# Performance work log

Hardware: AMD Instinct MI355X
Metric: run time of the kernel (lower is better)

Reference implementation:

```python
import jax, jax.numpy as jnp
import numpy as np

N_NODES = 100_000
N_EDGES = 600_000
D = 128


def setup_inputs() -> dict:
    key = jax.random.key(0)
    ks = jax.random.split(key, 8)
    x = jax.random.normal(ks[0], (N_NODES, D), dtype=jnp.float32)
    edge_index = jax.random.randint(ks[1], (2, N_EDGES), 0, N_NODES, dtype=jnp.int32)
    s = 1.0 / np.sqrt(D)
    Wn = jax.random.normal(ks[2], (D, D), dtype=jnp.float32) * s
    bn = jax.random.normal(ks[3], (D,), dtype=jnp.float32) * s
    We = jax.random.normal(ks[4], (D, 2 * D), dtype=jnp.float32) * s
    be = jax.random.normal(ks[5], (D,), dtype=jnp.float32) * s
    Wu = jax.random.normal(ks[6], (D, 3 * D), dtype=jnp.float32) * s
    bu = jax.random.normal(ks[7], (D,), dtype=jnp.float32) * s
    return {"x": x, "edge_index": edge_index, "Wn": Wn, "bn": bn,
            "We": We, "be": be, "Wu": Wu, "bu": bu}


def reference(x, edge_index, Wn, bn, We, be, Wu, bu):
    # x: [N, D] node embeddings; edge_index: [2, E]
    n = x.shape[0]
    src, dst = edge_index[0], edge_index[1]
    # node linear: [N, D]
    node_emb = x @ Wn.T + bn
    # edge linear on concatenated endpoint embeddings: [E, D]
    edge_in = jnp.concatenate([x[src], x[dst]], axis=1)  # [E, 2D]
    edge_emb = edge_in @ We.T + be
    # scatter-add neighbor node embeddings and edge embeddings into source nodes
    agg_node = jax.ops.segment_sum(node_emb[dst], src, num_segments=n)  # [N, D]
    agg_edge = jax.ops.segment_sum(edge_emb, src, num_segments=n)       # [N, D]
    pre = jnp.concatenate([node_emb, agg_node, agg_edge], axis=1)       # [N, 3D]
    # exact (erf) GELU matches torch nn.GELU default
    return jax.nn.gelu(pre, approximate=False) @ Wu.T + bu
```

## Files before the change

kernel.cpp:

```cpp
#include <hip/hip_runtime.h>
#include <hip/hip_bf16.h>
#include <math.h>

#define NNODES 100000
#define NEDGES 600000
#define DD 128
#define SCAN_B 512
#define NFRAGS 6250
#define TGRID 512

typedef __attribute__((ext_vector_type(8))) short bf16x8;
typedef __attribute__((ext_vector_type(4))) float f32x4;
typedef __attribute__((ext_vector_type(4))) unsigned short u16x4;

static __device__ __forceinline__ unsigned short f2bf(float f) {
    __hip_bfloat16 h = __float2bfloat16(f);
    return __builtin_bit_cast(unsigned short, h);
}
static __device__ __forceinline__ float bf2f(unsigned short h) {
    unsigned u = ((unsigned)h) << 16;
    return __builtin_bit_cast(float, u);
}
static __device__ __forceinline__ float gelu_fast(float v) {
    float w = v * (-2.302203846f - 0.102943150f * v * v);
#if __has_builtin(__builtin_amdgcn_exp2f)
    float e = __builtin_amdgcn_exp2f(w);
#else
    float e = exp2f(w);
#endif
#if __has_builtin(__builtin_amdgcn_rcpf)
    return v * __builtin_amdgcn_rcpf(1.0f + e);
#else
    return v / (1.0f + e);
#endif
}

#if __has_builtin(__builtin_amdgcn_global_load_lds)
#define HAVE_GLDS 1
#else
#define HAVE_GLDS 0
#endif

static __device__ __forceinline__ void gload_lds16(const unsigned short* g, unsigned short* s, int lane) {
#if HAVE_GLDS
    (void)lane;
    __builtin_amdgcn_global_load_lds((const __attribute__((address_space(1))) void*)g,
                                     (__attribute__((address_space(3))) void*)s, 16, 0, 0);
#else
    *(bf16x8*)(s + lane * 8) = *(const bf16x8*)g;
#endif
}
static __device__ __forceinline__ void gload_lds4(const float* g, unsigned short* s, int lane) {
#if HAVE_GLDS
    (void)lane;
    __builtin_amdgcn_global_load_lds((const __attribute__((address_space(1))) void*)g,
                                     (__attribute__((address_space(3))) void*)s, 4, 0, 0);
#else
    *(float*)((char*)s + lane * 4) = *g;
#endif
}

#define MFMA(a, b, c) __builtin_amdgcn_mfma_f32_16x16x32_bf16(a, b, c, 0, 0, 0)
#define BARX() do { asm volatile("s_waitcnt lgkmcnt(0)" ::: "memory"); \
                    __builtin_amdgcn_s_barrier(); } while (0)

template <int LAYOUT>
__global__ __launch_bounds__(256) void prep_k(const float* __restrict__ x,
                                              const float* __restrict__ Wn,
                                              const float* __restrict__ We,
                                              const float* __restrict__ Wu,
                                              unsigned short* __restrict__ wfrag,
                                              int* __restrict__ cnt,
                                              unsigned short* __restrict__ xb) {
    int b = blockIdx.x;
    int t = threadIdx.x;
    if (b < 48) {
        int tid = b * 256 + t;
        int l = tid & 63;
        const float* src;
        if constexpr (LAYOUT == 0) {
            int ct = (tid >> 6) & 7;
            int kt = (tid >> 9) & 3;
            int tile = tid >> 11;
            int n = ct * 16 + (l & 15);
            int k = kt * 32 + (l >> 4) * 8;
            switch (tile) {
                case 0:  src = Wn + (size_t)n * 128 + k;        break;
                case 1:  src = Wu + (size_t)n * 384 + k;        break;
                case 2:  src = We + (size_t)n * 256 + k;        break;
                case 3:  src = We + (size_t)n * 256 + 128 + k;  break;
                case 4:  src = Wu + (size_t)n * 384 + 128 + k;  break;
                default: src = Wu + (size_t)n * 384 + 256 + k;  break;
            }
        } else {
            int g = tid >> 6;
            int l16 = l & 15, lg8 = (l >> 4) * 8;
            if (g < 32)       { int nf = g >> 2,        kt = g & 3;
                                src = Wn + (size_t)(nf * 16 + l16) * 128 + kt * 32 + lg8; }
            else if (g < 64)  { int gg = g - 32; int nf = gg >> 2, kt = gg & 3;
                                src = We + (size_t)(nf * 16 + l16) * 256 + kt * 32 + lg8; }
            else if (g < 96)  { int gg = g - 64; int nf = gg >> 2, kt = gg & 3;
                                src = We + (size_t)(nf * 16 + l16) * 256 + 128 + kt * 32 + lg8; }
            else              { int gg = g - 96; int nf = gg / 12, kt = gg % 12;
                                src = Wu + (size_t)(nf * 16 + l16) * 384 + kt * 32 + lg8; }
        }
        unsigned short o[8];
#pragma unroll
        for (int j = 0; j < 8; ++j) o[j] = f2bf(src[j]);
        *(bf16x8*)(wfrag + (size_t)(b * 256 + t) * 8) = *(bf16x8*)o;
    } else if (b < 48 + 391) {
        int i = (b - 48) * 256 + t;
        if (i < NNODES) cnt[i] = 0;
    } else {
        int i = (b - 439) * 256 + t;
        float4 v0 = *(const float4*)(x + (size_t)i * 8);
        float4 v1 = *(const float4*)(x + (size_t)i * 8 + 4);
        unsigned short o[8] = { f2bf(v0.x), f2bf(v0.y), f2bf(v0.z), f2bf(v0.w),
                                f2bf(v1.x), f2bf(v1.y), f2bf(v1.z), f2bf(v1.w) };
        *(bf16x8*)(xb + (size_t)i * 8) = *(bf16x8*)o;
    }
}

__global__ __launch_bounds__(256) void hist_k(const int* __restrict__ ei, int* __restrict__ cnt) {
    int e = blockIdx.x * 256 + threadIdx.x;
    if (e < NEDGES) atomicAdd(&cnt[ei[e]], 1);
}

__global__ __launch_bounds__(SCAN_B) void scan_local(const int* __restrict__ cnt,
                                                     int* __restrict__ off,
                                                     int* __restrict__ bsum) {
    __shared__ int sh[SCAN_B];
    int i = blockIdx.x * SCAN_B + threadIdx.x;
    int v = (i < NNODES) ? cnt[i] : 0;
    sh[threadIdx.x] = v;
    __syncthreads();
    for (int d = 1; d < SCAN_B; d <<= 1) {
        int t = (threadIdx.x >= d) ? sh[threadIdx.x - d] : 0;
        __syncthreads();
        sh[threadIdx.x] += t;
        __syncthreads();
    }
    if (i < NNODES) off[i] = sh[threadIdx.x] - v;
    if (threadIdx.x == SCAN_B - 1) bsum[blockIdx.x] = sh[threadIdx.x];
}

__global__ __launch_bounds__(256) void scan_add2(int* __restrict__ off,
                                                 const int* __restrict__ bsum,
                                                 const int* __restrict__ cnt,
                                                 float* __restrict__ degf) {
    __shared__ int sp;
    int K = blockIdx.x >> 1;
    int t = threadIdx.x;
    if (t < 64) {
        int s = 0;
        for (int j = t; j < K; j += 64) s += bsum[j];
#pragma unroll
        for (int d = 32; d; d >>= 1) s += __shfl_down(s, d, 64);
        if (t == 0) sp = s;
    }
    __syncthreads();
    int i = blockIdx.x * 256 + t;
    if (i < NNODES) {
        off[i] += sp;
        degf[i] = (float)cnt[i];
    }
}

__global__ __launch_bounds__(256) void fill_k(const int* __restrict__ ei,
                                              int* __restrict__ off,
                                              int* __restrict__ edst) {
    int e = blockIdx.x * 256 + threadIdx.x;
    if (e >= NEDGES) return;
    int s = ei[e], d = ei[NEDGES + e];
    int pos = atomicAdd(&off[s], 1);
    edst[pos] = d;
}

template <bool IN_BF, bool OUT_BF>
__global__ __launch_bounds__(256) void agg2_k(const int* __restrict__ off,
                                              const int* __restrict__ edst,
                                              const float* __restrict__ xf,
                                              const unsigned short* __restrict__ xb,
                                              float* Sf, unsigned short* Sb) {
    int node = (blockIdx.x * 256 + threadIdx.x) >> 6;
    if (node >= NNODES) return;
    int l = threadIdx.x & 63;
    int es = l >> 4;
    int cg = l & 15;
    int end = off[node];
    int beg = node ? off[node - 1] : 0;
    float acc[8] = {0.f, 0.f, 0.f, 0.f, 0.f, 0.f, 0.f, 0.f};
    for (int e = beg + es; e < end; e += 4) {
        int d = edst[e];
        if constexpr (IN_BF) {
            bf16x8 v = *(const bf16x8*)(xb + (size_t)d * DD + cg * 8);
#pragma unroll
            for (int j = 0; j < 8; ++j) acc[j] += bf2f((unsigned short)v[j]);
        } else {
            const float* p = xf + (size_t)d * DD + cg * 8;
            float4 v0 = *(const float4*)(p);
            float4 v1 = *(const float4*)(p + 4);
            acc[0] += v0.x; acc[1] += v0.y; acc[2] += v0.z; acc[3] += v0.w;
            acc[4] += v1.x; acc[5] += v1.y; acc[6] += v1.z; acc[7] += v1.w;
        }
    }
#pragma unroll
    for (int j = 0; j < 8; ++j) {
        acc[j] += __shfl_xor(acc[j], 16, 64);
        acc[j] += __shfl_xor(acc[j], 32, 64);
    }
    if (es == 0) {
        if constexpr (OUT_BF) {
            unsigned short o[8];
#pragma unroll
            for (int j = 0; j < 8; ++j) o[j] = f2bf(acc[j]);
            *(bf16x8*)(Sb + (size_t)node * DD + cg * 8) = *(bf16x8*)o;
        } else {
            float4 r0 = { acc[0], acc[1], acc[2], acc[3] };
            float4 r1 = { acc[4], acc[5], acc[6], acc[7] };
            *(float4*)(Sf + (size_t)node * DD + cg * 8) = r0;
            *(float4*)(Sf + (size_t)node * DD + cg * 8 + 4) = r1;
        }
    }
}

__global__ __launch_bounds__(512, 2) void fusedT_k(const unsigned short* __restrict__ xb,
                                                   const unsigned short* __restrict__ Sb,
                                                   const float* __restrict__ degf,
                                                   const unsigned short* __restrict__ wfrag,
                                                   const float* __restrict__ bn,
                                                   const float* __restrict__ be,
                                                   const float* __restrict__ bu,
                                                   float* __restrict__ out) {
    __shared__ __align__(16) unsigned short XS[3][4224];
    __shared__ __align__(16) unsigned short Gs[2][6144];

    const int t = threadIdx.x;
    const int w = t >> 6;
    const int l = t & 63;
    const int l16 = l & 15;
    const int lg = l >> 4;
    const int sw = (l16 & 7) << 4;

    bf16x8 wn[4], we1[4], we2[4], wu[12];
#pragma unroll
    for (int kt = 0; kt < 4; ++kt) {
        wn[kt]  = *(const bf16x8*)(wfrag + (size_t)((w * 4 + kt) << 9) + l * 8);
        we1[kt] = *(const bf16x8*)(wfrag + (size_t)((32 + w * 4 + kt) << 9) + l * 8);
        we2[kt] = *(const bf16x8*)(wfrag + (size_t)((64 + w * 4 + kt) << 9) + l * 8);
    }
#pragma unroll
    for (int j = 0; j < 12; ++j)
        wu[j] = *(const bf16x8*)(wfrag + (size_t)((96 + w * 12 + j) << 9) + l * 8);
    f32x4 bnr = *(const f32x4*)(bn + w * 16 + lg * 4);
    f32x4 ber = *(const f32x4*)(be + w * 16 + lg * 4);
    f32x4 bur = *(const f32x4*)(bu + w * 16 + lg * 4);

    const int f0 = blockIdx.x;
    const int nIters = (NFRAGS - f0 + TGRID - 1) / TGRID;

    auto issueB = [&](int f, int buf) {
        int fc = (f < NFRAGS) ? f : (NFRAGS - 1);
        int p  = (w << 10) + (l << 4);
        int po = p & 4095;
        int q  = po ^ (((po >> 8) & 7) << 4);
        const unsigned short* base = (w < 4) ? xb : Sb;
        const unsigned short* src = base + (size_t)fc * 2048 + (q >> 1);
        unsigned short* dst = &XS[buf][(size_t)w << 9];
        gload_lds16(src, dst, l);
        gload_lds4(degf + fc * 16 + l16, &XS[buf][4096], l);
    };

    auto gemm1_epi = [&](const unsigned short* xs, unsigned short* gsw) {
        const char* xsb = (const char*)xs;
        bf16x8 bx[4], bs[4];
#pragma unroll
        for (int kt = 0; kt < 4; ++kt) {
            int po = (l16 << 8) + (kt << 6) + (lg << 4);
            bx[kt] = *(const bf16x8*)(xsb + (po ^ sw));
            bs[kt] = *(const bf16x8*)(xsb + 4096 + (po ^ sw));
        }
        float dg = *(const float*)(xsb + 8192 + l16 * 4);
        f32x4 a0 = {0.f,0.f,0.f,0.f}, a1 = a0, a2 = a0, a3 = a0;
        __builtin_amdgcn_s_setprio(1);
#pragma unroll
        for (int kt = 0; kt < 4; ++kt) {
            a0 = MFMA(wn[kt],  bx[kt], a0);
            a1 = MFMA(wn[kt],  bs[kt], a1);
            a2 = MFMA(we1[kt], bx[kt], a2);
            a3 = MFMA(we2[kt], bs[kt], a3);
        }
        __builtin_amdgcn_s_setprio(0);
        u16x4 g0, g1, g2;
#pragma unroll
        for (int r = 0; r < 4; ++r) {
            g0[r] = f2bf(gelu_fast(a0[r] + bnr[r]));
            g1[r] = f2bf(gelu_fast(a1[r] + dg * bnr[r]));
            g2[r] = f2bf(gelu_fast(dg * (a2[r] + ber[r]) + a3[r]));
        }
        char* gb = (char*)gsw;
        int cb = w * 32 + lg * 8;
        *(u16x4*)(gb + ((l16 * 768 + cb)       ^ sw)) = g0;
        *(u16x4*)(gb + ((l16 * 768 + 256 + cb) ^ sw)) = g1;
        *(u16x4*)(gb + ((l16 * 768 + 512 + cb) ^ sw)) = g2;
    };

    auto gemm2_store = [&](int f, const unsigned short* gsr) {
        const char* gb = (const char*)gsr;
        f32x4 o = {0.f, 0.f, 0.f, 0.f};
        __builtin_amdgcn_s_setprio(1);
#pragma unroll
        for (int j = 0; j < 12; ++j) {
            bf16x8 g = *(const bf16x8*)(gb + ((l16 * 768 + j * 64 + lg * 16) ^ sw));
            o = MFMA(wu[j], g, o);
        }
        __builtin_amdgcn_s_setprio(0);
        int v = f * 16 + l16;
        float4 st = { o[0] + bur[0], o[1] + bur[1], o[2] + bur[2], o[3] + bur[3] };
        *(float4*)(out + (size_t)v * DD + w * 16 + lg * 4) = st;
    };

    issueB(f0, 0);
    issueB(f0 + TGRID, 1);

    issueB(f0 + 2 * TGRID, 2);
    asm volatile("s_waitcnt vmcnt(4)" ::: "memory");
    BARX();
    gemm1_epi(&XS[0][0], &Gs[0][0]);
    BARX();

    gemm2_store(f0, &Gs[0][0]);
    issueB(f0 + 3 * TGRID, 0);
    asm volatile("s_waitcnt vmcnt(4)" ::: "memory");
    BARX();
    gemm1_epi(&XS[1][0], &Gs[1][0]);
    BARX();

    for (int i = 2; i < nIters; ++i) {
        gemm2_store(f0 + (i - 1) * TGRID, &Gs[(i - 1) & 1][0]);
        issueB(f0 + (i + 2) * TGRID, (i + 2) % 3);
        asm volatile("s_waitcnt vmcnt(4)" ::: "memory");
        BARX();
        gemm1_epi(&XS[i % 3][0], &Gs[i & 1][0]);
        BARX();
    }
    gemm2_store(f0 + (nIters - 1) * TGRID, &Gs[(nIters - 1) & 1][0]);
}

#define PREQ(q) do { \
    if ((q) <= 20)      asm volatile("s_waitcnt vmcnt(3)" ::: "memory"); \
    else if ((q) == 21) asm volatile("s_waitcnt vmcnt(2)" ::: "memory"); \
    else if ((q) == 22) asm volatile("s_waitcnt vmcnt(1)" ::: "memory"); \
    else                asm volatile("s_waitcnt vmcnt(0)" ::: "memory"); \
    asm volatile("s_waitcnt lgkmcnt(0)" ::: "memory"); \
    __builtin_amdgcn_s_barrier(); \
    if ((q) + 4 < 24) issue_q((q) + 4); } while (0)

template <int MODE>
__global__ __launch_bounds__(512) void fused4_k(const float* __restrict__ xf,
                                                const unsigned short* __restrict__ xb,
                                                const float* Sf,
                                                const float* __restrict__ degf,
                                                const unsigned short* __restrict__ wfrag,
                                                const float* __restrict__ bn,
                                                const float* __restrict__ be,
                                                const float* __restrict__ bu,
                                                float* out) {
    extern __shared__ char smem[];
    unsigned short* Q  = (unsigned short*)smem;
    unsigned short* Gs = Q + 5 * 4096;
    float* degs = (float*)(Gs + 128 * 136);

    const int t = threadIdx.x;
    const int w = t >> 6;
    const int l = t & 63;
    const int wc = w & 1;
    const int rb = (w >> 1) * 32;
    const int l16 = l & 15;
    const int lg = l >> 4;
    const int node0 = blockIdx.x * 128;

    int r0 = node0 + rb + l16;      if (r0 > NNODES - 1) r0 = NNODES - 1;
    int r1 = node0 + rb + 16 + l16; if (r1 > NNODES - 1) r1 = NNODES - 1;

    auto loadA_bf = [&](const unsigned short* rowp, bf16x8 (&A)[4][2], int f) {
#pragma unroll
        for (int kt = 0; kt < 4; ++kt)
            A[kt][f] = *(const bf16x8*)(rowp + kt * 32 + lg * 8);
    };
    auto loadA_f32 = [&](const float* rowp, bf16x8 (&A)[4][2], int f) {
#pragma unroll
        for (int kt = 0; kt < 4; ++kt) {
            const float* p = rowp + kt * 32 + lg * 8;
            float4 v0 = *(const float4*)(p);
            float4 v1 = *(const float4*)(p + 4);
            bf16x8 a;
            a[0] = (short)f2bf(v0.x); a[1] = (short)f2bf(v0.y);
            a[2] = (short)f2bf(v0.z); a[3] = (short)f2bf(v0.w);
            a[4] = (short)f2bf(v1.x); a[5] = (short)f2bf(v1.y);
            a[6] = (short)f2bf(v1.z); a[7] = (short)f2bf(v1.w);
            A[kt][f] = a;
        }
    };

    bf16x8 aX[4][2], aS[4][2];
    if constexpr (MODE >= 1) {
        loadA_bf(xb + (size_t)r0 * DD, aX, 0);
        loadA_bf(xb + (size_t)r1 * DD, aX, 1);
    } else {
        loadA_f32(xf + (size_t)r0 * DD, aX, 0);
        loadA_f32(xf + (size_t)r1 * DD, aX, 1);
    }
    loadA_f32(Sf + (size_t)r0 * DD, aS, 0);
    loadA_f32(Sf + (size_t)r1 * DD, aS, 1);
    float bnc[4], bec[4], buc[4];
#pragma unroll
    for (int c = 0; c < 4; ++c) {
        int col = (wc * 4 + c) * 16 + l16;
        bnc[c] = bn[col]; bec[c] = be[col]; buc[c] = bu[col];
    }
    if (t < 128) {
        int gr = node0 + t;
        degs[t] = (gr < NNODES) ? degf[gr] : 0.f;
    }

    auto issue_q = [&](int q) {
        const unsigned short* src = wfrag + (size_t)q * 4096 + w * 512 + l * 8;
        unsigned short* dst = Q + (q % 5) * 4096 + w * 512;
        gload_lds16(src, dst, l);
    };
    issue_q(0); issue_q(1); issue_q(2); issue_q(3);

    f32x4 zz = { 0.f, 0.f, 0.f, 0.f };
    f32x4 acc1[2][4], acc2[2][4], acc3[2][4], accO[2][4];
#pragma unroll
    for (int f = 0; f < 2; ++f)
#pragma unroll
        for (int c = 0; c < 4; ++c) {
            acc1[f][c] = zz; acc2[f][c] = zz; acc3[f][c] = zz; accO[f][c] = zz;
        }

    auto bload = [&](int q5, int c) -> bf16x8 {
        return *(const bf16x8*)(Q + q5 * 4096 + (wc * 4 + c) * 512 + l * 8);
    };
    auto body_wn = [&](int kt, int q5) {
        __builtin_amdgcn_s_setprio(1);
#pragma unroll
        for (int c = 0; c < 4; ++c) {
            bf16x8 b = bload(q5, c);
            acc1[0][c] = MFMA(aX[kt][0], b, acc1[0][c]);
            acc1[1][c] = MFMA(aX[kt][1], b, acc1[1][c]);
            acc2[0][c] = MFMA(aS[kt][0], b, acc2[0][c]);
            acc2[1][c] = MFMA(aS[kt][1], b, acc2[1][c]);
        }
        __builtin_amdgcn_s_setprio(0);
    };
    auto body_A = [&](int kt, int q5, bf16x8 (&A)[4][2], f32x4 (&acc)[2][4]) {
        __builtin_amdgcn_s_setprio(1);
#pragma unroll
        for (int c = 0; c < 4; ++c) {
            bf16x8 b = bload(q5, c);
            acc[0][c] = MFMA(A[kt][0], b, acc[0][c]);
            acc[1][c] = MFMA(A[kt][1], b, acc[1][c]);
        }
        __builtin_amdgcn_s_setprio(0);
    };
    auto body_wu = [&](int kt, int q5) {
        bf16x8 g0 = *(const bf16x8*)(Gs + (rb + l16) * 136 + kt * 32 + lg * 8);
        bf16x8 g1 = *(const bf16x8*)(Gs + (rb + 16 + l16) * 136 + kt * 32 + lg * 8);
        __builtin_amdgcn_s_setprio(1);
#pragma unroll
        for (int c = 0; c < 4; ++c) {
            bf16x8 b = bload(q5, c);
            accO[0][c] = MFMA(g0, b, accO[0][c]);
            accO[1][c] = MFMA(g1, b, accO[1][c]);
        }
        __builtin_amdgcn_s_setprio(0);
    };

    float dg[2][4];
    auto epi = [&](f32x4 (&acc)[2][4], const float* bias, int degMode) {
#pragma unroll
        for (int f = 0; f < 2; ++f)
#pragma unroll
            for (int c = 0; c < 4; ++c) {
                int col = (wc * 4 + c) * 16 + l16;
#pragma unroll
                for (int r = 0; r < 4; ++r) {
                    int row = rb + f * 16 + lg * 4 + r;
                    float v = acc[f][c][r];
                    if (degMode == 0) v += bias[c];
                    if (degMode == 1) v += dg[f][r] * bias[c];
                    Gs[row * 136 + col] = f2bf(gelu_fast(v));
                }
            }
    };
    auto fold3 = [&] {
#pragma unroll
        for (int f = 0; f < 2; ++f)
#pragma unroll
            for (int c = 0; c < 4; ++c)
#pragma unroll
                for (int r = 0; r < 4; ++r)
                    acc3[f][c][r] = dg[f][r] * (acc3[f][c][r] + bec[c]);
    };

    PREQ(0);
#pragma unroll
    for (int f = 0; f < 2; ++f)
#pragma unroll
        for (int r = 0; r < 4; ++r)
            dg[f][r] = degs[rb + f * 16 + lg * 4 + r];
    body_wn(0, 0);
    PREQ(1);  body_wn(1, 1);
    PREQ(2);  body_wn(2, 2);
    PREQ(3);  body_wn(3, 3);
    PREQ(4);  epi(acc1, bnc, 0); BARX(); body_wu(0, 4);
    PREQ(5);  body_wu(1, 0);
    PREQ(6);  body_wu(2, 1);
    PREQ(7);  body_wu(3, 2);
    PREQ(8);  body_A(0, 3, aX, acc3);
    PREQ(9);  body_A(1, 4, aX, acc3);
    PREQ(10); body_A(2, 0, aX, acc3);
    PREQ(11); body_A(3, 1, aX, acc3);
    fold3();
    PREQ(12); body_A(0, 2, aS, acc3);
    PREQ(13); body_A(1, 3, aS, acc3);
    PREQ(14); body_A(2, 4, aS, acc3);
    PREQ(15); body_A(3, 0, aS, acc3);
    PREQ(16); epi(acc2, bnc, 1); BARX(); body_wu(0, 1);
    PREQ(17); body_wu(1, 2);
    PREQ(18); body_wu(2, 3);
    PREQ(19); body_wu(3, 4);
    PREQ(20); epi(acc3, nullptr, 2); BARX(); body_wu(0, 0);
    PREQ(21); body_wu(1, 1);
    PREQ(22); body_wu(2, 2);
    PREQ(23); body_wu(3, 3);

#pragma unroll
    for (int f = 0; f < 2; ++f)
#pragma unroll
        for (int c = 0; c < 4; ++c) {
            int col = (wc * 4 + c) * 16 + l16;
#pragma unroll
            for (int r = 0; r < 4; ++r) {
                int grow = node0 + rb + f * 16 + lg * 4 + r;
                if (grow < NNODES)
                    out[(size_t)grow * DD + col] = accO[f][c][r] + buc[c];
            }
        }
}

extern "C" void kernel_launch(void* const* d_in, const int* in_sizes, int n_in,
                              void* d_out, int out_size, void* d_ws, size_t ws_size,
                              hipStream_t stream) {
    const float* x  = (const float*)d_in[0];
    const int*   ei = (const int*)d_in[1];
    const float* Wn = (const float*)d_in[2];
    const float* bn = (const float*)d_in[3];
    const float* We = (const float*)d_in[4];
    const float* be = (const float*)d_in[5];
    const float* Wu = (const float*)d_in[6];
    const float* bu = (const float*)d_in[7];

    float* out = (float*)d_out;

    unsigned short* wfrag = (unsigned short*)d_ws;
    float* degf = (float*)((char*)d_ws + 196608);
    int* cnt  = (int*)((char*)d_ws + 596608);
    int* off  = (int*)((char*)d_ws + 996608);
    int* bsum = (int*)((char*)d_ws + 1396608);
    int* edst = (int*)((char*)d_ws + 1398656);
    unsigned short* xbf = (unsigned short*)((char*)d_ws + 3798656);
    unsigned short* Sbf = (unsigned short*)((char*)d_ws + 29398656);

    int mode = 0;
    if (ws_size >= 29398656ULL + 25600000ULL) mode = 2;
    else if (ws_size >= 3798656ULL + 25600000ULL) mode = 1;

    int nb = (NNODES + SCAN_B - 1) / SCAN_B;
    int pblocks = (mode >= 1) ? (439 + NNODES * DD / 8 / 256) : 439;

    if (mode == 2) {
        prep_k<1><<<pblocks, 256, 0, stream>>>(x, Wn, We, Wu, wfrag, cnt, xbf);
        hist_k<<<(NEDGES + 255) / 256, 256, 0, stream>>>(ei, cnt);
        scan_local<<<nb, SCAN_B, 0, stream>>>(cnt, off, bsum);
        scan_add2<<<(NNODES + 255) / 256, 256, 0, stream>>>(off, bsum, cnt, degf);
        fill_k<<<(NEDGES + 255) / 256, 256, 0, stream>>>(ei, off, edst);
        agg2_k<true, true><<<NNODES / 4, 256, 0, stream>>>(off, edst, x, xbf, nullptr, Sbf);
        fusedT_k<<<TGRID, 512, 0, stream>>>(xbf, Sbf, degf, wfrag, bn, be, bu, out);
    } else {
        prep_k<0><<<pblocks, 256, 0, stream>>>(x, Wn, We, Wu, wfrag, cnt, xbf);
        hist_k<<<(NEDGES + 255) / 256, 256, 0, stream>>>(ei, cnt);
        scan_local<<<nb, SCAN_B, 0, stream>>>(cnt, off, bsum);
        scan_add2<<<(NNODES + 255) / 256, 256, 0, stream>>>(off, bsum, cnt, degf);
        fill_k<<<(NEDGES + 255) / 256, 256, 0, stream>>>(ei, off, edst);
        int fblocks = (NNODES + 127) / 128;
        size_t lds_bytes = 5 * 4096 * 2 + 128 * 136 * 2 + 128 * 4;
        if (mode == 1) {
            agg2_k<true, false><<<NNODES / 4, 256, 0, stream>>>(off, edst, x, xbf, out, nullptr);
            fused4_k<1><<<fblocks, 512, lds_bytes, stream>>>(x, xbf, out, degf, wfrag,
                                                             bn, be, bu, out);
        } else {
            agg2_k<false, false><<<NNODES / 4, 256, 0, stream>>>(off, edst, x, nullptr, out, nullptr);
            fused4_k<0><<<fblocks, 512, lds_bytes, stream>>>(x, nullptr, out, degf, wfrag,
                                                             bn, be, bu, out);
        }
    }
}
```

Baseline: 162.1 us.

## Fuse histogram into prep kernel, dual-accumulate gather and split GEMM2 chains

The mode-2 path now zeroes the degree counters with a memset and folds the edge histogram into the prep kernel, which drops one kernel launch and lets the histogram atomics overlap with the weight and x conversions. The gather loop in the aggregation kernel handles two edges per iteration with separate accumulators to keep more loads in flight. The second GEMM splits its 12-step MFMA dependency chain into three independent accumulators to hide MFMA latency. The memset and merged kernel depend on stream ordering for correctness, and the extra accumulators raise register use.

```diff
diff --git a/kernel.cpp b/kernel.cpp
--- a/kernel.cpp
+++ b/kernel.cpp
@@ -8,6 +8,10 @@
 #define SCAN_B 512
 #define NFRAGS 6250
 #define TGRID 512
+
+#define P1_W 48
+#define P1_X (P1_W + 6250)
+#define P1_H (P1_X + (NEDGES + 255) / 256)
 
 typedef __attribute__((ext_vector_type(8))) short bf16x8;
 typedef __attribute__((ext_vector_type(4))) float f32x4;
@@ -64,60 +68,91 @@
 #define BARX() do { asm volatile("s_waitcnt lgkmcnt(0)" ::: "memory"); \
                     __builtin_amdgcn_s_barrier(); } while (0)
 
-template <int LAYOUT>
-__global__ __launch_bounds__(256) void prep_k(const float* __restrict__ x,
-                                              const float* __restrict__ Wn,
-                                              const float* __restrict__ We,
-                                              const float* __restrict__ Wu,
-                                              unsigned short* __restrict__ wfrag,
-                                              int* __restrict__ cnt,
-                                              unsigned short* __restrict__ xb) {
+__global__ __launch_bounds__(256) void prep1_k(const float* __restrict__ x,
+                                               const float* __restrict__ Wn,
+                                               const float* __restrict__ We,
+                                               const float* __restrict__ Wu,
+                                               const int* __restrict__ ei,
+                                               unsigned short* __restrict__ wfrag,
+                                               int* __restrict__ cnt,
+                                               unsigned short* __restrict__ xb) {
+    int b = blockIdx.x;
+    int t = threadIdx.x;
+    if (b < P1_W) {
+        int tid = b * 256 + t;
+        int l = tid & 63;
+        int g = tid >> 6;
+        int l16 = l & 15, lg8 = (l >> 4) * 8;
+        const float* src;
+        if (g < 32)       { int nf = g >> 2,        kt = g & 3;
+                            src = Wn + (size_t)(nf * 16 + l16) * 128 + kt * 32 + lg8; }
+        else if (g < 64)  { int gg = g - 32; int nf = gg >> 2, kt = gg & 3;
+                            src = We + (size_t)(nf * 16 + l16) * 256 + kt * 32 + lg8; }
+        else if (g < 96)  { int gg = g - 64; int nf = gg >> 2, kt = gg & 3;
+                            src = We + (size_t)(nf * 16 + l16) * 256 + 128 + kt * 32 + lg8; }
+        else              { int gg = g - 96; int nf = gg / 12, kt = gg % 12;
+                            src = Wu + (size_t)(nf * 16 + l16) * 384 + kt * 32 + lg8; }
+        unsigned short o[8];
+#pragma unroll
+        for (int j = 0; j < 8; ++j) o[j] = f2bf(src[j]);
+        *(bf16x8*)(wfrag + (size_t)tid * 8) = *(bf16x8*)o;
+    } else if (b < P1_X) {
+        int i = (b - P1_W) * 256 + t;
+        if (i < NNODES * DD / 8) {
+            float4 v0 = *(const float4*)(x + (size_t)i * 8);
+            float4 v1 = *(const float4*)(x + (size_t)i * 8 + 4);
+            unsigned short o[8] = { f2bf(v0.x), f2bf(v0.y), f2bf(v0.z), f2bf(v0.w),
+                                    f2bf(v1.x), f2bf(v1.y), f2bf(v1.z), f2bf(v1.w) };
+            *(bf16x8*)(xb + (size_t)i * 8) = *(bf16x8*)o;
+        }
+    } else {
+        int e = (b - P1_X) * 256 + t;
+        if (e < NEDGES) atomicAdd(&cnt[ei[e]], 1);
+    }
+}
+
+__global__ __launch_bounds__(256) void prep0_k(const float* __restrict__ x,
+                                               const float* __restrict__ Wn,
+                                               const float* __restrict__ We,
+                                               const float* __restrict__ Wu,
+                                               unsigned short* __restrict__ wfrag,
+                                               int* __restrict__ cnt,
+                                               unsigned short* __restrict__ xb) {
     int b = blockIdx.x;
     int t = threadIdx.x;
     if (b < 48) {
         int tid = b * 256 + t;
         int l = tid & 63;
+        int ct = (tid >> 6) & 7;
+        int kt = (tid >> 9) & 3;
+        int tile = tid >> 11;
+        int n = ct * 16 + (l & 15);
+        int k = kt * 32 + (l >> 4) * 8;
         const float* src;
-        if constexpr (LAYOUT == 0) {
-            int ct = (tid >> 6) & 7;
-            int kt = (tid >> 9) & 3;
-            int tile = tid >> 11;
-            int n = ct * 16 + (l & 15);
-            int k = kt * 32 + (l >> 4) * 8;
-            switch (tile) {
-                case 0:  src = Wn + (size_t)n * 128 + k;        break;
-                case 1:  src = Wu + (size_t)n * 384 + k;        break;
-                case 2:  src = We + (size_t)n * 256 + k;        break;
-                case 3:  src = We + (size_t)n * 256 + 128 + k;  break;
-                case 4:  src = Wu + (size_t)n * 384 + 128 + k;  break;
-                default: src = Wu + (size_t)n * 384 + 256 + k;  break;
-            }
-        } else {
-            int g = tid >> 6;
-            int l16 = l & 15, lg8 = (l >> 4) * 8;
-            if (g < 32)       { int nf = g >> 2,        kt = g & 3;
-                                src = Wn + (size_t)(nf * 16 + l16) * 128 + kt * 32 + lg8; }
-            else if (g < 64)  { int gg = g - 32; int nf = gg >> 2, kt = gg & 3;
-                                src = We + (size_t)(nf * 16 + l16) * 256 + kt * 32 + lg8; }
-            else if (g < 96)  { int gg = g - 64; int nf = gg >> 2, kt = gg & 3;
-                                src = We + (size_t)(nf * 16 + l16) * 256 + 128 + kt * 32 + lg8; }
-            else              { int gg = g - 96; int nf = gg / 12, kt = gg % 12;
-                                src = Wu + (size_t)(nf * 16 + l16) * 384 + kt * 32 + lg8; }
+        switch (tile) {
+            case 0:  src = Wn + (size_t)n * 128 + k;        break;
+            case 1:  src = Wu + (size_t)n * 384 + k;        break;
+            case 2:  src = We + (size_t)n * 256 + k;        break;
+            case 3:  src = We + (size_t)n * 256 + 128 + k;  break;
+            case 4:  src = Wu + (size_t)n * 384 + 128 + k;  break;
+            default: src = Wu + (size_t)n * 384 + 256 + k;  break;
         }
         unsigned short o[8];
 #pragma unroll
         for (int j = 0; j < 8; ++j) o[j] = f2bf(src[j]);
-        *(bf16x8*)(wfrag + (size_t)(b * 256 + t) * 8) = *(bf16x8*)o;
+        *(bf16x8*)(wfrag + (size_t)tid * 8) = *(bf16x8*)o;
     } else if (b < 48 + 391) {
         int i = (b - 48) * 256 + t;
         if (i < NNODES) cnt[i] = 0;
     } else {
         int i = (b - 439) * 256 + t;
-        float4 v0 = *(const float4*)(x + (size_t)i * 8);
-        float4 v1 = *(const float4*)(x + (size_t)i * 8 + 4);
-        unsigned short o[8] = { f2bf(v0.x), f2bf(v0.y), f2bf(v0.z), f2bf(v0.w),
-                                f2bf(v1.x), f2bf(v1.y), f2bf(v1.z), f2bf(v1.w) };
-        *(bf16x8*)(xb + (size_t)i * 8) = *(bf16x8*)o;
+        if (i < NNODES * DD / 8) {
+            float4 v0 = *(const float4*)(x + (size_t)i * 8);
+            float4 v1 = *(const float4*)(x + (size_t)i * 8 + 4);
+            unsigned short o[8] = { f2bf(v0.x), f2bf(v0.y), f2bf(v0.z), f2bf(v0.w),
+                                    f2bf(v1.x), f2bf(v1.y), f2bf(v1.z), f2bf(v1.w) };
+            *(bf16x8*)(xb + (size_t)i * 8) = *(bf16x8*)o;
+        }
     }
 }
 
@@ -190,22 +225,46 @@
     int end = off[node];
     int beg = node ? off[node - 1] : 0;
     float acc[8] = {0.f, 0.f, 0.f, 0.f, 0.f, 0.f, 0.f, 0.f};
-    for (int e = beg + es; e < end; e += 4) {
-        int d = edst[e];
+    float acc2[8] = {0.f, 0.f, 0.f, 0.f, 0.f, 0.f, 0.f, 0.f};
+    int e = beg + es;
+    for (; e + 4 < end; e += 8) {
+        int d0 = edst[e];
+        int d1 = edst[e + 4];
         if constexpr (IN_BF) {
-            bf16x8 v = *(const bf16x8*)(xb + (size_t)d * DD + cg * 8);
-#pragma unroll
-            for (int j = 0; j < 8; ++j) acc[j] += bf2f((unsigned short)v[j]);
+            bf16x8 v0 = *(const bf16x8*)(xb + (size_t)d0 * DD + cg * 8);
+            bf16x8 v1 = *(const bf16x8*)(xb + (size_t)d1 * DD + cg * 8);
+#pragma unroll
+            for (int j = 0; j < 8; ++j) {
+                acc[j]  += bf2f((unsigned short)v0[j]);
+                acc2[j] += bf2f((unsigned short)v1[j]);
+            }
         } else {
-            const float* p = xf + (size_t)d * DD + cg * 8;
-            float4 v0 = *(const float4*)(p);
-            float4 v1 = *(const float4*)(p + 4);
-            acc[0] += v0.x; acc[1] += v0.y; acc[2] += v0.z; acc[3] += v0.w;
-            acc[4] += v1.x; acc[5] += v1.y; acc[6] += v1.z; acc[7] += v1.w;
+            const float* p0 = xf + (size_t)d0 * DD + cg * 8;
+            const float* p1 = xf + (size_t)d1 * DD + cg * 8;
+            float4 a0 = *(const float4*)(p0), a1 = *(const float4*)(p0 + 4);
+            float4 b0 = *(const float4*)(p1), b1 = *(const float4*)(p1 + 4);
+            acc[0] += a0.x; acc[1] += a0.y; acc[2] += a0.z; acc[3] += a0.w;
+            acc[4] += a1.x; acc[5] += a1.y; acc[6] += a1.z; acc[7] += a1.w;
+            acc2[0] += b0.x; acc2[1] += b0.y; acc2[2] += b0.z; acc2[3] += b0.w;
+            acc2[4] += b1.x; acc2[5] += b1.y; acc2[6] += b1.z; acc2[7] += b1.w;
+        }
+    }
+    if (e < end) {
+        int d0 = edst[e];
+        if constexpr (IN_BF) {
+            bf16x8 v0 = *(const bf16x8*)(xb + (size_t)d0 * DD + cg * 8);
+#pragma unroll
+            for (int j = 0; j < 8; ++j) acc[j] += bf2f((unsigned short)v0[j]);
+        } else {
+            const float* p0 = xf + (size_t)d0 * DD + cg * 8;
+            float4 a0 = *(const float4*)(p0), a1 = *(const float4*)(p0 + 4);
+            acc[0] += a0.x; acc[1] += a0.y; acc[2] += a0.z; acc[3] += a0.w;
+            acc[4] += a1.x; acc[5] += a1.y; acc[6] += a1.z; acc[7] += a1.w;
         }
     }
 #pragma unroll
     for (int j = 0; j < 8; ++j) {
+        acc[j] += acc2[j];
         acc[j] += __shfl_xor(acc[j], 16, 64);
         acc[j] += __shfl_xor(acc[j], 32, 64);
     }
@@ -307,14 +366,19 @@
 
     auto gemm2_store = [&](int f, const unsigned short* gsr) {
         const char* gb = (const char*)gsr;
-        f32x4 o = {0.f, 0.f, 0.f, 0.f};
+        f32x4 o0 = {0.f, 0.f, 0.f, 0.f}, o1 = o0, o2 = o0;
         __builtin_amdgcn_s_setprio(1);
 #pragma unroll
-        for (int j = 0; j < 12; ++j) {
-            bf16x8 g = *(const bf16x8*)(gb + ((l16 * 768 + j * 64 + lg * 16) ^ sw));
-            o = MFMA(wu[j], g, o);
+        for (int j = 0; j < 4; ++j) {
+            bf16x8 ga = *(const bf16x8*)(gb + ((l16 * 768 + (3*j+0) * 64 + lg * 16) ^ sw));
+            bf16x8 gc = *(const bf16x8*)(gb + ((l16 * 768 + (3*j+1) * 64 + lg * 16) ^ sw));
+            bf16x8 ge = *(const bf16x8*)(gb + ((l16 * 768 + (3*j+2) * 64 + lg * 16) ^ sw));
+            o0 = MFMA(wu[3*j+0], ga, o0);
+            o1 = MFMA(wu[3*j+1], gc, o1);
+            o2 = MFMA(wu[3*j+2], ge, o2);
         }
         __builtin_amdgcn_s_setprio(0);
+        f32x4 o = (o0 + o1) + o2;
         int v = f * 16 + l16;
         float4 st = { o[0] + bur[0], o[1] + bur[1], o[2] + bur[2], o[3] + bur[3] };
         *(float4*)(out + (size_t)v * DD + w * 16 + lg * 4) = st;
@@ -579,18 +643,18 @@
     else if (ws_size >= 3798656ULL + 25600000ULL) mode = 1;
 
     int nb = (NNODES + SCAN_B - 1) / SCAN_B;
-    int pblocks = (mode >= 1) ? (439 + NNODES * DD / 8 / 256) : 439;
 
     if (mode == 2) {
-        prep_k<1><<<pblocks, 256, 0, stream>>>(x, Wn, We, Wu, wfrag, cnt, xbf);
-        hist_k<<<(NEDGES + 255) / 256, 256, 0, stream>>>(ei, cnt);
+        hipMemsetAsync(cnt, 0, (size_t)NNODES * sizeof(int), stream);
+        prep1_k<<<P1_H, 256, 0, stream>>>(x, Wn, We, Wu, ei, wfrag, cnt, xbf);
         scan_local<<<nb, SCAN_B, 0, stream>>>(cnt, off, bsum);
         scan_add2<<<(NNODES + 255) / 256, 256, 0, stream>>>(off, bsum, cnt, degf);
         fill_k<<<(NEDGES + 255) / 256, 256, 0, stream>>>(ei, off, edst);
         agg2_k<true, true><<<NNODES / 4, 256, 0, stream>>>(off, edst, x, xbf, nullptr, Sbf);
         fusedT_k<<<TGRID, 512, 0, stream>>>(xbf, Sbf, degf, wfrag, bn, be, bu, out);
     } else {
-        prep_k<0><<<pblocks, 256, 0, stream>>>(x, Wn, We, Wu, wfrag, cnt, xbf);
+        int pblocks = (mode >= 1) ? (439 + NNODES * DD / 8 / 256 + 1) : 439;
+        prep0_k<<<pblocks, 256, 0, stream>>>(x, Wn, We, Wu, wfrag, cnt, xbf);
         hist_k<<<(NEDGES + 255) / 256, 256, 0, stream>>>(ei, cnt);
         scan_local<<<nb, SCAN_B, 0, stream>>>(cnt, off, bsum);
         scan_add2<<<(NNODES + 255) / 256, 256, 0, stream>>>(off, bsum, cnt, degf);
```

New measurement: 163.3 us. Within noise of the previous version (+0.7%).
